# Kernel tuning notes

Measured on AMD Instinct MI355X. Metric: run time of the kernel, lower is better.

The kernel has to match this reference:

```python
import jax, jax.numpy as jnp
import numpy as np

B, T, TR, DIM, H = 1, 4096, 1024, 1536, 12
DH = DIM // H          # 128
EPS = 1e-6             # RMSNorm eps
REF_SCALE = 1.0


def setup_inputs() -> dict:
    key = jax.random.key(0)
    ks = jax.random.split(key, 20)
    s = 0.02
    w = lambda k: jax.random.normal(k, (DIM, DIM), jnp.float32) * s
    b = lambda k: jax.random.normal(k, (DIM,), jnp.float32) * 0.01
    theta = jax.random.uniform(ks[2], (T, DH // 2), jnp.float32) * (2.0 * np.pi)
    return {
        "hidden_states": jax.random.normal(ks[0], (B, T, DIM), jnp.float32),
        "ref_hidden_states": jax.random.normal(ks[1], (B, TR, DIM), jnp.float32),
        "rot_cos": jnp.cos(theta),
        "rot_sin": jnp.sin(theta),
        "Wq": w(ks[3]), "bq": b(ks[4]),
        "Wk": w(ks[5]), "bk": b(ks[6]),
        "Wv": w(ks[7]), "bv": b(ks[8]),
        "Wkr": w(ks[9]), "bkr": b(ks[10]),
        "Wvr": w(ks[11]), "bvr": b(ks[12]),
        "Wo": w(ks[13]), "bo": b(ks[14]),
        "gq": jnp.ones((DIM,), jnp.float32),
        "gk": jnp.ones((DIM,), jnp.float32),
    }


def _rmsnorm(x, g):
    return x * jax.lax.rsqrt(jnp.mean(x * x, axis=-1, keepdims=True) + EPS) * g


def _heads(x):  # [B, T, DIM] -> [B, H, T, DH]
    return x.reshape(B, -1, H, DH).transpose(0, 2, 1, 3)


def _merge(x):  # [B, H, T, DH] -> [B, T, DIM]
    return x.transpose(0, 2, 1, 3).reshape(B, -1, DIM)


def _rope(x, c, s):
    # consecutive pairs along DH form complex numbers (view_as_complex semantics)
    xe, xo = x[..., 0::2], x[..., 1::2]
    c = c[None, None]  # [1,1,T,DH/2]
    s = s[None, None]
    re = xe * c - xo * s
    im = xe * s + xo * c
    return jnp.stack([re, im], axis=-1).reshape(x.shape)


def _attn(q, k, v):
    scale = 1.0 / jnp.sqrt(jnp.asarray(DH, q.dtype))
    p = jax.nn.softmax(jnp.einsum("bhqd,bhkd->bhqk", q, k) * scale, axis=-1)
    return jnp.einsum("bhqk,bhkd->bhqd", p, v)


def reference(hidden_states, ref_hidden_states, rot_cos, rot_sin,
              Wq, bq, Wk, bk, Wv, bv, Wkr, bkr, Wvr, bvr, Wo, bo, gq, gk):
    # QKV projections (self-attention: encoder_hidden_states = hidden_states)
    q_lin = hidden_states @ Wq + bq
    k_lin = hidden_states @ Wk + bk
    v_lin = hidden_states @ Wv + bv

    # ---- reference-attention branch (uses pre-RoPE query) ----
    ref_q = _heads(_rmsnorm(q_lin, gq))
    ref_k = _heads(_rmsnorm(ref_hidden_states @ Wkr + bkr, gk))
    ref_v = _heads(ref_hidden_states @ Wvr + bvr)
    ref_out = _merge(_attn(ref_q, ref_k, ref_v))  # [B, T, DIM]

    # ---- main attention with QK-norm + RoPE ----
    q = _rope(_heads(_rmsnorm(q_lin, gq)), rot_cos, rot_sin)
    k = _rope(_heads(_rmsnorm(k_lin, gk)), rot_cos, rot_sin)
    v = _heads(v_lin)
    main_out = _merge(_attn(q, k, v))  # [B, T, DIM]

    # scaled residual combine + output projection (dropout = identity)
    out = main_out + REF_SCALE * ref_out
    return out @ Wo + bo
```

## Files before the change

kernel.cpp:

```cpp
#include <hip/hip_runtime.h>

typedef unsigned short u16;
typedef unsigned int u32;
typedef __attribute__((ext_vector_type(8))) short short8;
typedef __attribute__((ext_vector_type(4))) float f32x4;

__device__ inline u16 f2b(float f) {
  u32 u = __builtin_bit_cast(u32, f);
  u += 0x7fff + ((u >> 16) & 1);
  return (u16)(u >> 16);
}
__device__ inline float b2f(u16 u) {
  return __builtin_bit_cast(float, (u32)u << 16);
}
__device__ inline u32 pack_bf16_rn(float a, float b) {
  const u32 ua = __builtin_bit_cast(u32, a) + 0x8000u;
  const u32 ub = __builtin_bit_cast(u32, b) + 0x8000u;
  return (ua >> 16) | (ub & 0xffff0000u);
}
__device__ inline void c_store(float* p, float v) { *p = v; }
__device__ inline void c_store(u16* p, float v) { *p = f2b(v); }

__device__ inline float fexp2(float x) {
#if __has_builtin(__builtin_amdgcn_exp2f)
  return __builtin_amdgcn_exp2f(x);
#else
  return exp2f(x);
#endif
}

typedef const __attribute__((address_space(1))) u32 gu32;
typedef __attribute__((address_space(3))) u32 lu32;
__device__ inline void async16(const u16* g, u16* l) {
  __builtin_amdgcn_global_load_lds((gu32*)g, (lu32*)l, 16, 0, 0);
}

#define QS (0.08838834764831843f * 1.4426950408889634f)

template <int MI, typename TC>
__global__ __launch_bounds__(256) void gemm128_kernel(
    const u16* __restrict__ A, long lda,
    const u16* __restrict__ Bt, long ldb,
    TC* __restrict__ C0, TC* __restrict__ C1, TC* __restrict__ C2, long ldc,
    const float* b0, const float* b1, const float* b2,
    int K) {
  __shared__ u16 As[32 * MI * 32];
  __shared__ u16 Bs[128 * 32];

  const int tid = threadIdx.x;
  const int lane = tid & 63;
  const int w = tid >> 6;
  const int r = lane & 15;
  const int quad = lane >> 4;
  const int m0 = blockIdx.y * (32 * MI);
  const int nb = blockIdx.x * 128;
  const int seg = nb / 1536;
  const int nc = nb - seg * 1536;
  TC* C = seg == 0 ? C0 : (seg == 1 ? C1 : C2);
  const float* bias = seg == 0 ? b0 : (seg == 1 ? b1 : b2);

  const int srow = lane >> 2;
  const int sx = ((lane & 3) ^ (srow & 3)) * 8;
  const u16* Ag = A + (size_t)(m0 + w * 8 * MI + srow) * lda + sx;
  const u16* Bg = Bt + (size_t)(nb + w * 32 + srow) * ldb + sx;
  u16* Al[MI / 2];
#pragma unroll
  for (int j = 0; j < MI / 2; ++j) Al[j] = &As[(w * 8 * MI + 16 * j) * 32];
  u16* const Bl0 = &Bs[(w * 32) * 32];
  u16* const Bl1 = &Bs[(w * 32 + 16) * 32];

  const int wm = (w >> 1) * (16 * MI);
  const int wn = (w & 1) * 64;

  f32x4 acc[MI][4];
#pragma unroll
  for (int i = 0; i < MI; ++i)
#pragma unroll
    for (int j = 0; j < 4; ++j) acc[i][j] = (f32x4){0.f, 0.f, 0.f, 0.f};

  const int fco = (quad ^ (r & 3)) * 8;

  for (int kk = 0; kk < K; kk += 32) {
    __syncthreads();
#pragma unroll
    for (int j = 0; j < MI / 2; ++j) async16(Ag + kk + (size_t)(16 * j) * lda, Al[j]);
    async16(Bg + kk, Bl0);
    async16(Bg + kk + 16 * ldb, Bl1);
    __syncthreads();

    short8 af[MI], bf[4];
#pragma unroll
    for (int mi = 0; mi < MI; ++mi)
      af[mi] = *reinterpret_cast<const short8*>(&As[(wm + 16 * mi + r) * 32 + fco]);
#pragma unroll
    for (int ni = 0; ni < 4; ++ni)
      bf[ni] = *reinterpret_cast<const short8*>(&Bs[(wn + 16 * ni + r) * 32 + fco]);
#pragma unroll
    for (int mi = 0; mi < MI; ++mi)
#pragma unroll
      for (int ni = 0; ni < 4; ++ni)
        acc[mi][ni] = __builtin_amdgcn_mfma_f32_16x16x32_bf16(af[mi], bf[ni], acc[mi][ni], 0, 0, 0);
  }

#pragma unroll
  for (int mi = 0; mi < MI; ++mi)
#pragma unroll
    for (int ni = 0; ni < 4; ++ni)
#pragma unroll
      for (int rr = 0; rr < 4; ++rr) {
        const int row = m0 + wm + 16 * mi + 4 * quad + rr;
        const int col = nc + wn + 16 * ni + r;
        c_store(&C[(size_t)row * ldc + col], acc[mi][ni][rr] + bias[col]);
      }
}

__global__ __launch_bounds__(256) void conv2_kernel(
    const float* __restrict__ xa, u16* __restrict__ ya, int n8a,
    const float* __restrict__ xb, u16* __restrict__ yb, int n8b) {
  int i = blockIdx.x * 256 + threadIdx.x;
  const float* x;
  u16* y;
  if (i < n8a) {
    x = xa; y = ya;
  } else {
    i -= n8a;
    if (i >= n8b) return;
    x = xb; y = yb;
  }
  const float4 v0 = reinterpret_cast<const float4*>(x)[2 * i];
  const float4 v1 = reinterpret_cast<const float4*>(x)[2 * i + 1];
  uint4 rv;
  rv.x = (u32)f2b(v0.x) | ((u32)f2b(v0.y) << 16);
  rv.y = (u32)f2b(v0.z) | ((u32)f2b(v0.w) << 16);
  rv.z = (u32)f2b(v1.x) | ((u32)f2b(v1.y) << 16);
  rv.w = (u32)f2b(v1.z) | ((u32)f2b(v1.w) << 16);
  reinterpret_cast<uint4*>(y)[i] = rv;
}

__device__ inline void transconv_body(const float* __restrict__ W, u16* __restrict__ Wt) {
  __shared__ u16 Ls[64 * 72];
  const int tid = threadIdx.x;
  const int k0 = blockIdx.y * 64;
  const int n0 = blockIdx.x * 64;
#pragma unroll
  for (int i = 0; i < 4; ++i) {
    const int c = tid + 256 * i;
    const int row = c >> 4;
    const int c4 = (c & 15) * 4;
    const float4 v = *reinterpret_cast<const float4*>(&W[(size_t)(k0 + row) * 1536 + n0 + c4]);
    Ls[(c4 + 0) * 72 + row] = f2b(v.x);
    Ls[(c4 + 1) * 72 + row] = f2b(v.y);
    Ls[(c4 + 2) * 72 + row] = f2b(v.z);
    Ls[(c4 + 3) * 72 + row] = f2b(v.w);
  }
  __syncthreads();
#pragma unroll
  for (int i = 0; i < 2; ++i) {
    const int c = tid + 256 * i;
    const int n = c >> 3;
    const int kc = (c & 7) * 8;
    u16 tmp[8];
#pragma unroll
    for (int j = 0; j < 8; ++j) tmp[j] = Ls[n * 72 + kc + j];
    *reinterpret_cast<uint4*>(&Wt[(size_t)(n0 + n) * 1536 + k0 + kc]) =
        *reinterpret_cast<const uint4*>(tmp);
  }
}

__global__ __launch_bounds__(256) void transconv6_kernel(
    const float* W0, const float* W1, const float* W2,
    const float* W3, const float* W4, const float* W5,
    u16* T0, u16* T1, u16* T2, u16* T3, u16* T4, u16* T5) {
  const int z = blockIdx.z;
  const float* W = z == 0 ? W0 : z == 1 ? W1 : z == 2 ? W2 : z == 3 ? W3 : z == 4 ? W4 : W5;
  u16* Wt = z == 0 ? T0 : z == 1 ? T1 : z == 2 ? T2 : z == 3 ? T3 : z == 4 ? T4 : T5;
  transconv_body(W, Wt);
}

__global__ __launch_bounds__(256) void rmsnorm3_kernel(
    const u16* xq, const u16* xk, const u16* xkr,
    const float* gq, const float* gk,
    const float* rc, const float* rs,
    u16* oq_plain, u16* oq_rope, u16* ok_rope, u16* okr_plain) {
  __shared__ float red[4];
  const int z = blockIdx.y;
  const int row = blockIdx.x;
  if (z == 2 && row >= 1024) return;
  const u16* x; const float* g; u16* po; u16* pr; float sc;
  if (z == 0)      { x = xq;  g = gq; po = oq_plain; pr = oq_rope; sc = QS;  }
  else if (z == 1) { x = xk;  g = gk; po = nullptr;  pr = ok_rope; sc = 1.f; }
  else             { x = xkr; g = gk; po = okr_plain; pr = nullptr; sc = 1.f; }

  const int tid = threadIdx.x;
  const u32* xr = reinterpret_cast<const u32*>(x + (size_t)row * 1536);
  float xe[3], xo[3];
  float ss = 0.f;
#pragma unroll
  for (int j = 0; j < 3; ++j) {
    const u32 u = xr[tid + 256 * j];
    const float e = b2f((u16)(u & 0xffff));
    const float o = b2f((u16)(u >> 16));
    xe[j] = e; xo[j] = o;
    ss += e * e + o * o;
  }
#pragma unroll
  for (int off = 32; off; off >>= 1) ss += __shfl_xor(ss, off, 64);
  if ((tid & 63) == 0) red[tid >> 6] = ss;
  __syncthreads();
  const float total = red[0] + red[1] + red[2] + red[3];
  const float rinv = rsqrtf(total * (1.0f / 1536.0f) + 1e-6f) * sc;
  u32* po32 = po ? reinterpret_cast<u32*>(po + (size_t)row * 1536) : nullptr;
  u32* pr32 = pr ? reinterpret_cast<u32*>(pr + (size_t)row * 1536) : nullptr;
#pragma unroll
  for (int j = 0; j < 3; ++j) {
    const int p = tid + 256 * j;
    const float2 gg = reinterpret_cast<const float2*>(g)[p];
    const float e = xe[j] * rinv * gg.x;
    const float o = xo[j] * rinv * gg.y;
    if (po32) po32[p] = (u32)f2b(e) | ((u32)f2b(o) << 16);
    if (pr32) {
      const int i = p & 63;
      const float c = rc[row * 64 + i];
      const float s = rs[row * 64 + i];
      const float re = e * c - o * s;
      const float im = e * s + o * c;
      pr32[p] = (u32)f2b(re) | ((u32)f2b(im) << 16);
    }
  }
}

__global__ __launch_bounds__(256) void vtrans2_kernel(
    const u16* __restrict__ V0, u16* __restrict__ Vt0,
    const u16* __restrict__ V1, u16* __restrict__ Vt1) {
  __shared__ u16 Ls[64 * 136];
  const int z = blockIdx.z;
  const int kvLen = z == 0 ? 4096 : 1024;
  const int kv0 = blockIdx.x * 64;
  if (kv0 >= kvLen) return;
  const u16* V = z == 0 ? V0 : V1;
  u16* Vt = z == 0 ? Vt0 : Vt1;
  const int tid = threadIdx.x;
  const int h = blockIdx.y;
#pragma unroll
  for (int i = 0; i < 4; ++i) {
    const int c = tid + 256 * i;
    const int row = c >> 4, c8 = c & 15;
    *reinterpret_cast<uint4*>(&Ls[row * 136 + 8 * c8]) =
        *reinterpret_cast<const uint4*>(V + (size_t)(kv0 + row) * 1536 + h * 128 + 8 * c8);
  }
  __syncthreads();
#pragma unroll
  for (int i = 0; i < 4; ++i) {
    const int c = tid + 256 * i;
    const int d = c >> 3, kc = c & 7;
    u16 tmp[8];
#pragma unroll
    for (int j = 0; j < 8; ++j) tmp[j] = Ls[(8 * kc + j) * 136 + d];
    *reinterpret_cast<uint4*>(Vt + ((size_t)h * 128 + d) * kvLen + kv0 + 8 * kc) =
        *reinterpret_cast<const uint4*>(tmp);
  }
}

__global__ __launch_bounds__(256, 4) void flash_kernel(
    const u16* __restrict__ Qc, const u16* __restrict__ Kc,
    const u16* __restrict__ Vc, int kvLenC,
    const u16* __restrict__ Qm, const u16* __restrict__ Km,
    const u16* __restrict__ Vm, int kvLenM,
    u16* __restrict__ Ob) {
  __shared__ u16 Ks[2][32 * 128];
  __shared__ u16 Vs[2][128 * 32];
  __shared__ u16 Pb[4][16 * 40];
  __shared__ float ab[4][16];

  const int tid = threadIdx.x;
  const int lane = tid & 63;
  const int w = tid >> 6;
  const int r = lane & 15;
  const int quad = lane >> 4;
  const int h = blockIdx.y;
  const int q0 = blockIdx.x * 64;
  const int qrow = q0 + 16 * w + r;
  const int fv = (r >> 1) & 3;

  auto run_pass = [&](const u16* __restrict__ Q, const u16* __restrict__ K,
                      const u16* __restrict__ Vt, int kvLen, f32x4* Oc) {
    short8 qf[4];
    {
      const u16* qbase = Q + (size_t)qrow * 1536 + h * 128 + 8 * quad;
#pragma unroll
      for (int ks = 0; ks < 4; ++ks)
        qf[ks] = *reinterpret_cast<const short8*>(qbase + 32 * ks);
    }

    const u16* Kb = K + h * 128;
    const u16* Vb = Vt + (size_t)h * 128 * kvLen;
    u32 koff[2], voff[2];
    int klo[2], vlo[2];
    {
      const int p16 = lane & 15, rin = lane >> 4;
      const int p4 = lane & 3, din = lane >> 2;
#pragma unroll
      for (int j = 0; j < 2; ++j) {
        const int row = 8 * w + 4 * j + rin;
        koff[j] = (u32)row * 1536u + 8u * (u32)(p16 ^ (row & 15));
        klo[j] = (8 * w + 4 * j) * 128;
        const int d = 32 * w + 16 * j + din;
        voff[j] = (u32)d * (u32)kvLen + 8u * (u32)(p4 ^ ((din >> 1) & 3));
        vlo[j] = (32 * w + 16 * j) * 32;
      }
    }

#pragma unroll
    for (int dt = 0; dt < 8; ++dt) Oc[dt] = (f32x4){0.f, 0.f, 0.f, 0.f};
    float m_i = -1e30f, l_i = 0.f;

    const int nt = kvLen >> 5;

#pragma unroll
    for (int j = 0; j < 2; ++j) async16(Kb + koff[j], &Ks[0][klo[j]]);
#pragma unroll
    for (int j = 0; j < 2; ++j) async16(Vb + voff[j], &Vs[0][vlo[j]]);

    for (int t = 0; t < nt; ++t) {
      const int buf = t & 1;
      __syncthreads();
      if (t + 1 < nt) {
        const size_t ko = (size_t)(t + 1) * (32 * 1536);
        const size_t vo = (size_t)(t + 1) * 32;
#pragma unroll
        for (int j = 0; j < 2; ++j) async16(Kb + ko + koff[j], &Ks[buf ^ 1][klo[j]]);
#pragma unroll
        for (int j = 0; j < 2; ++j) async16(Vb + vo + voff[j], &Vs[buf ^ 1][vlo[j]]);
      }

      f32x4 St[2];
#pragma unroll
      for (int mt = 0; mt < 2; ++mt) St[mt] = (f32x4){0.f, 0.f, 0.f, 0.f};
      __builtin_amdgcn_s_setprio(1);
#pragma unroll
      for (int mt = 0; mt < 2; ++mt) {
        const u16* kp = &Ks[buf][(16 * mt + r) * 128];
#pragma unroll
        for (int ks = 0; ks < 4; ++ks) {
          const short8 af = *reinterpret_cast<const short8*>(kp + 8 * ((quad + 4 * ks) ^ r));
          St[mt] = __builtin_amdgcn_mfma_f32_16x16x32_bf16(af, qf[ks], St[mt], 0, 0, 0);
        }
      }
      __builtin_amdgcn_s_setprio(0);

      float mloc = -1e30f;
#pragma unroll
      for (int mt = 0; mt < 2; ++mt)
#pragma unroll
        for (int rr = 0; rr < 4; ++rr) mloc = fmaxf(mloc, St[mt][rr]);
      mloc = fmaxf(mloc, __shfl_xor(mloc, 16, 64));
      mloc = fmaxf(mloc, __shfl_xor(mloc, 32, 64));

      float alpha = 1.0f;
      if (__any(mloc > m_i + 11.5f)) {
        const float mn = fmaxf(m_i, mloc);
        alpha = fexp2(m_i - mn);
        m_i = mn;
        if (quad == 0) ab[w][r] = alpha;
        const float4 a4 = *reinterpret_cast<const float4*>(&ab[w][4 * quad]);
#pragma unroll
        for (int dt = 0; dt < 8; ++dt) {
          Oc[dt][0] *= a4.x; Oc[dt][1] *= a4.y; Oc[dt][2] *= a4.z; Oc[dt][3] *= a4.w;
        }
      }

      float psum = 0.f;
      uint2 pk[2];
#pragma unroll
      for (int mt = 0; mt < 2; ++mt) {
        const float p0 = fexp2(St[mt][0] - m_i);
        const float p1 = fexp2(St[mt][1] - m_i);
        const float p2 = fexp2(St[mt][2] - m_i);
        const float p3 = fexp2(St[mt][3] - m_i);
        psum += (p0 + p1) + (p2 + p3);
        pk[mt].x = pack_bf16_rn(p0, p1);
        pk[mt].y = pack_bf16_rn(p2, p3);
      }
      psum += __shfl_xor(psum, 16, 64);
      psum += __shfl_xor(psum, 32, 64);
      l_i = l_i * alpha + psum;

#pragma unroll
      for (int mt = 0; mt < 2; ++mt)
        *reinterpret_cast<uint2*>(&Pb[w][r * 40 + 16 * mt + 4 * quad]) = pk[mt];
      {
        const short8 pa = *reinterpret_cast<const short8*>(&Pb[w][r * 40 + 8 * quad]);
        __builtin_amdgcn_s_setprio(1);
#pragma unroll
        for (int dt = 0; dt < 8; ++dt) {
          const int d = 16 * dt + r;
          const short8 b0 = *reinterpret_cast<const short8*>(&Vs[buf][d * 32 + 8 * (quad ^ fv)]);
          Oc[dt] = __builtin_amdgcn_mfma_f32_16x16x32_bf16(pa, b0, Oc[dt], 0, 0, 0);
        }
        __builtin_amdgcn_s_setprio(0);
      }
    }

    if (quad == 0) ab[w][r] = 1.0f / l_i;
    const float4 li4 = *reinterpret_cast<const float4*>(&ab[w][4 * quad]);
#pragma unroll
    for (int dt = 0; dt < 8; ++dt) {
      Oc[dt][0] *= li4.x; Oc[dt][1] *= li4.y; Oc[dt][2] *= li4.z; Oc[dt][3] *= li4.w;
    }
  };

  f32x4 Ocr[8];
  run_pass(Qc, Kc, Vc, kvLenC, Ocr);
  __syncthreads();
  f32x4 Oc[8];
  run_pass(Qm, Km, Vm, kvLenM, Oc);

  u16* obb = Ob + (size_t)(q0 + 16 * w) * 1536 + h * 128;
#pragma unroll
  for (int rr = 0; rr < 4; ++rr) {
    u16* brow = obb + (size_t)(4 * quad + rr) * 1536 + r;
#pragma unroll
    for (int dt = 0; dt < 8; ++dt)
      brow[16 * dt] = f2b(Oc[dt][rr] + Ocr[dt][rr]);
  }
}

extern "C" void kernel_launch(void* const* d_in, const int* in_sizes, int n_in,
                              void* d_out, int out_size, void* d_ws, size_t ws_size,
                              hipStream_t stream) {
  (void)in_sizes; (void)n_in; (void)out_size; (void)ws_size;
  constexpr int T = 4096, TR = 1024, DIM = 1536, NH = 12;

  const float* hs  = (const float*)d_in[0];
  const float* rhs = (const float*)d_in[1];
  const float* rc  = (const float*)d_in[2];
  const float* rs  = (const float*)d_in[3];
  const float* Wq  = (const float*)d_in[4];
  const float* bq  = (const float*)d_in[5];
  const float* Wk  = (const float*)d_in[6];
  const float* bk  = (const float*)d_in[7];
  const float* Wv  = (const float*)d_in[8];
  const float* bv  = (const float*)d_in[9];
  const float* Wkr = (const float*)d_in[10];
  const float* bkr = (const float*)d_in[11];
  const float* Wvr = (const float*)d_in[12];
  const float* bvr = (const float*)d_in[13];
  const float* Wo  = (const float*)d_in[14];
  const float* bo  = (const float*)d_in[15];
  const float* gq  = (const float*)d_in[16];
  const float* gk  = (const float*)d_in[17];
  float* out = (float*)d_out;

  char* ws = (char*)d_ws;
  size_t off = 0;
  auto alloc = [&](size_t bytes) -> void* {
    void* p = ws + off;
    off += (bytes + 255) & ~(size_t)255;
    return p;
  };
  u16* bQ    = (u16*)alloc((size_t)T * DIM * 2);
  u16* bQr   = (u16*)alloc((size_t)T * DIM * 2);
  u16* bK    = (u16*)alloc((size_t)T * DIM * 2);
  u16* bV    = (u16*)alloc((size_t)T * DIM * 2);
  u16* bKr   = (u16*)alloc((size_t)TR * DIM * 2);
  u16* bVr   = (u16*)alloc((size_t)TR * DIM * 2);
  u16* bHs   = (u16*)alloc((size_t)T * DIM * 2);
  u16* bRhs  = (u16*)alloc((size_t)TR * DIM * 2);
  u16* bWqkv = (u16*)alloc((size_t)3 * DIM * DIM * 2);
  u16* bWr   = (u16*)alloc((size_t)2 * DIM * DIM * 2);
  u16* bWoT  = (u16*)alloc((size_t)DIM * DIM * 2);
  u16* VtG = bHs;
  u16* VtR = bRhs;
  u16* bOb = bWqkv;

  const dim3 blk(256);

  conv2_kernel<<<dim3((T * DIM / 8 + TR * DIM / 8 + 255) / 256), blk, 0, stream>>>(
      hs, bHs, T * DIM / 8, rhs, bRhs, TR * DIM / 8);

  transconv6_kernel<<<dim3(24, 24, 6), blk, 0, stream>>>(
      Wq, Wk, Wv, Wkr, Wvr, Wo,
      bWqkv + 0 * (size_t)DIM * DIM, bWqkv + 1 * (size_t)DIM * DIM,
      bWqkv + 2 * (size_t)DIM * DIM, bWr + 0 * (size_t)DIM * DIM,
      bWr + 1 * (size_t)DIM * DIM, bWoT);

  gemm128_kernel<4, u16><<<dim3(36, 32), blk, 0, stream>>>(
      bHs, DIM, bWqkv, DIM, bQ, bK, bV, DIM, bq, bk, bv, DIM);
  gemm128_kernel<2, u16><<<dim3(24, 16), blk, 0, stream>>>(
      bRhs, DIM, bWr, DIM, bKr, bVr, (u16*)nullptr, DIM, bkr, bvr, nullptr, DIM);

  rmsnorm3_kernel<<<dim3(T, 3), blk, 0, stream>>>(
      bQ, bK, bKr, gq, gk, rc, rs, bQ, bQr, bK, bKr);

  vtrans2_kernel<<<dim3(T / 64, NH, 2), blk, 0, stream>>>(bV, VtG, bVr, VtR);

  flash_kernel<<<dim3(T / 64, NH), blk, 0, stream>>>(
      bQ, bKr, VtR, TR, bQr, bK, VtG, T, bOb);

  gemm128_kernel<2, float><<<dim3(12, 64), blk, 0, stream>>>(
      bOb, DIM, bWoT, DIM, out, (float*)nullptr, (float*)nullptr, DIM, bo, nullptr, nullptr, DIM);
}
```

Baseline: 542.6 us.

## Process two query tiles per wave in flash kernel with 128-thread blocks

The flash attention block shrinks from four waves to two, and each wave now handles 32 query rows (two 16-row tiles). Each K/V fragment read from shared memory then feeds two MFMAs, which halves LDS traffic per unit of compute. The first pass writes its fp32 output to a new global scratch buffer, and the second pass reads it back to combine. This replaces holding two register accumulator sets and frees registers for the doubled tile. The cost is fewer waves per block, more global memory traffic for the fp32 intermediate, and more per-thread async loads.

```diff
diff --git a/kernel.cpp b/kernel.cpp
--- a/kernel.cpp
+++ b/kernel.cpp
@@ -261,15 +261,15 @@
   }
 }
 
-__global__ __launch_bounds__(256, 4) void flash_kernel(
+__global__ __launch_bounds__(128, 2) void flash_kernel(
     const u16* __restrict__ Qc, const u16* __restrict__ Kc,
     const u16* __restrict__ Vc, int kvLenC,
     const u16* __restrict__ Qm, const u16* __restrict__ Km,
     const u16* __restrict__ Vm, int kvLenM,
-    u16* __restrict__ Ob) {
+    float* __restrict__ O, u16* __restrict__ Ob) {
   __shared__ u16 Ks[2][32 * 128];
   __shared__ u16 Vs[2][128 * 32];
-  __shared__ u16 Pb[4][16 * 40];
+  __shared__ u16 Pb[2][32 * 40];
   __shared__ float ab[4][16];
 
   const int tid = threadIdx.x;
@@ -279,47 +279,50 @@
   const int quad = lane >> 4;
   const int h = blockIdx.y;
   const int q0 = blockIdx.x * 64;
-  const int qrow = q0 + 16 * w + r;
   const int fv = (r >> 1) & 3;
 
   auto run_pass = [&](const u16* __restrict__ Q, const u16* __restrict__ K,
-                      const u16* __restrict__ Vt, int kvLen, f32x4* Oc) {
-    short8 qf[4];
-    {
-      const u16* qbase = Q + (size_t)qrow * 1536 + h * 128 + 8 * quad;
+                      const u16* __restrict__ Vt, int kvLen, bool addO) {
+    short8 qf[2][4];
+#pragma unroll
+    for (int qt = 0; qt < 2; ++qt) {
+      const u16* qbase = Q + (size_t)(q0 + 32 * w + 16 * qt + r) * 1536 + h * 128 + 8 * quad;
 #pragma unroll
       for (int ks = 0; ks < 4; ++ks)
-        qf[ks] = *reinterpret_cast<const short8*>(qbase + 32 * ks);
+        qf[qt][ks] = *reinterpret_cast<const short8*>(qbase + 32 * ks);
     }
 
     const u16* Kb = K + h * 128;
     const u16* Vb = Vt + (size_t)h * 128 * kvLen;
-    u32 koff[2], voff[2];
-    int klo[2], vlo[2];
+    u32 koff[4], voff[4];
+    int klo[4], vlo[4];
     {
       const int p16 = lane & 15, rin = lane >> 4;
       const int p4 = lane & 3, din = lane >> 2;
 #pragma unroll
-      for (int j = 0; j < 2; ++j) {
-        const int row = 8 * w + 4 * j + rin;
+      for (int j = 0; j < 4; ++j) {
+        const int row = 16 * w + 4 * j + rin;
         koff[j] = (u32)row * 1536u + 8u * (u32)(p16 ^ (row & 15));
-        klo[j] = (8 * w + 4 * j) * 128;
-        const int d = 32 * w + 16 * j + din;
-        voff[j] = (u32)d * (u32)kvLen + 8u * (u32)(p4 ^ ((din >> 1) & 3));
-        vlo[j] = (32 * w + 16 * j) * 32;
+        klo[j] = (16 * w + 4 * j) * 128;
+        const int d = 64 * w + 16 * j + din;
+        voff[j] = (u32)d * (u32)kvLen + 8u * (u32)(p4 ^ ((d >> 1) & 3));
+        vlo[j] = (64 * w + 16 * j) * 32;
       }
     }
 
-#pragma unroll
-    for (int dt = 0; dt < 8; ++dt) Oc[dt] = (f32x4){0.f, 0.f, 0.f, 0.f};
-    float m_i = -1e30f, l_i = 0.f;
+    f32x4 Oc[2][8];
+#pragma unroll
+    for (int qt = 0; qt < 2; ++qt)
+#pragma unroll
+      for (int dt = 0; dt < 8; ++dt) Oc[qt][dt] = (f32x4){0.f, 0.f, 0.f, 0.f};
+    float m_i[2] = {-1e30f, -1e30f}, l_i[2] = {0.f, 0.f};
 
     const int nt = kvLen >> 5;
 
 #pragma unroll
-    for (int j = 0; j < 2; ++j) async16(Kb + koff[j], &Ks[0][klo[j]]);
-#pragma unroll
-    for (int j = 0; j < 2; ++j) async16(Vb + voff[j], &Vs[0][vlo[j]]);
+    for (int j = 0; j < 4; ++j) async16(Kb + koff[j], &Ks[0][klo[j]]);
+#pragma unroll
+    for (int j = 0; j < 4; ++j) async16(Vb + voff[j], &Vs[0][vlo[j]]);
 
     for (int t = 0; t < nt; ++t) {
       const int buf = t & 1;
@@ -328,14 +331,16 @@
         const size_t ko = (size_t)(t + 1) * (32 * 1536);
         const size_t vo = (size_t)(t + 1) * 32;
 #pragma unroll
-        for (int j = 0; j < 2; ++j) async16(Kb + ko + koff[j], &Ks[buf ^ 1][klo[j]]);
-#pragma unroll
-        for (int j = 0; j < 2; ++j) async16(Vb + vo + voff[j], &Vs[buf ^ 1][vlo[j]]);
-      }
-
-      f32x4 St[2];
-#pragma unroll
-      for (int mt = 0; mt < 2; ++mt) St[mt] = (f32x4){0.f, 0.f, 0.f, 0.f};
+        for (int j = 0; j < 4; ++j) async16(Kb + ko + koff[j], &Ks[buf ^ 1][klo[j]]);
+#pragma unroll
+        for (int j = 0; j < 4; ++j) async16(Vb + vo + voff[j], &Vs[buf ^ 1][vlo[j]]);
+      }
+
+      f32x4 St[2][2];
+#pragma unroll
+      for (int qt = 0; qt < 2; ++qt)
+#pragma unroll
+        for (int mt = 0; mt < 2; ++mt) St[qt][mt] = (f32x4){0.f, 0.f, 0.f, 0.f};
       __builtin_amdgcn_s_setprio(1);
 #pragma unroll
       for (int mt = 0; mt < 2; ++mt) {
@@ -343,86 +348,106 @@
 #pragma unroll
         for (int ks = 0; ks < 4; ++ks) {
           const short8 af = *reinterpret_cast<const short8*>(kp + 8 * ((quad + 4 * ks) ^ r));
-          St[mt] = __builtin_amdgcn_mfma_f32_16x16x32_bf16(af, qf[ks], St[mt], 0, 0, 0);
+#pragma unroll
+          for (int qt = 0; qt < 2; ++qt)
+            St[qt][mt] = __builtin_amdgcn_mfma_f32_16x16x32_bf16(af, qf[qt][ks], St[qt][mt], 0, 0, 0);
         }
       }
       __builtin_amdgcn_s_setprio(0);
 
-      float mloc = -1e30f;
-#pragma unroll
-      for (int mt = 0; mt < 2; ++mt)
-#pragma unroll
-        for (int rr = 0; rr < 4; ++rr) mloc = fmaxf(mloc, St[mt][rr]);
-      mloc = fmaxf(mloc, __shfl_xor(mloc, 16, 64));
-      mloc = fmaxf(mloc, __shfl_xor(mloc, 32, 64));
-
-      float alpha = 1.0f;
-      if (__any(mloc > m_i + 11.5f)) {
-        const float mn = fmaxf(m_i, mloc);
-        alpha = fexp2(m_i - mn);
-        m_i = mn;
-        if (quad == 0) ab[w][r] = alpha;
-        const float4 a4 = *reinterpret_cast<const float4*>(&ab[w][4 * quad]);
-#pragma unroll
-        for (int dt = 0; dt < 8; ++dt) {
-          Oc[dt][0] *= a4.x; Oc[dt][1] *= a4.y; Oc[dt][2] *= a4.z; Oc[dt][3] *= a4.w;
+      uint2 pk[2][2];
+#pragma unroll
+      for (int qt = 0; qt < 2; ++qt) {
+        float mloc = -1e30f;
+#pragma unroll
+        for (int mt = 0; mt < 2; ++mt)
+#pragma unroll
+          for (int rr = 0; rr < 4; ++rr) mloc = fmaxf(mloc, St[qt][mt][rr]);
+        mloc = fmaxf(mloc, __shfl_xor(mloc, 16, 64));
+        mloc = fmaxf(mloc, __shfl_xor(mloc, 32, 64));
+
+        float alpha = 1.0f;
+        if (__any(mloc > m_i[qt] + 11.5f)) {
+          const float mn = fmaxf(m_i[qt], mloc);
+          alpha = fexp2(m_i[qt] - mn);
+          m_i[qt] = mn;
+          if (quad == 0) ab[2 * w + qt][r] = alpha;
+          const float4 a4 = *reinterpret_cast<const float4*>(&ab[2 * w + qt][4 * quad]);
+#pragma unroll
+          for (int dt = 0; dt < 8; ++dt) {
+            Oc[qt][dt][0] *= a4.x; Oc[qt][dt][1] *= a4.y;
+            Oc[qt][dt][2] *= a4.z; Oc[qt][dt][3] *= a4.w;
+          }
         }
-      }
-
-      float psum = 0.f;
-      uint2 pk[2];
-#pragma unroll
-      for (int mt = 0; mt < 2; ++mt) {
-        const float p0 = fexp2(St[mt][0] - m_i);
-        const float p1 = fexp2(St[mt][1] - m_i);
-        const float p2 = fexp2(St[mt][2] - m_i);
-        const float p3 = fexp2(St[mt][3] - m_i);
-        psum += (p0 + p1) + (p2 + p3);
-        pk[mt].x = pack_bf16_rn(p0, p1);
-        pk[mt].y = pack_bf16_rn(p2, p3);
-      }
-      psum += __shfl_xor(psum, 16, 64);
-      psum += __shfl_xor(psum, 32, 64);
-      l_i = l_i * alpha + psum;
-
-#pragma unroll
-      for (int mt = 0; mt < 2; ++mt)
-        *reinterpret_cast<uint2*>(&Pb[w][r * 40 + 16 * mt + 4 * quad]) = pk[mt];
+
+        float psum = 0.f;
+#pragma unroll
+        for (int mt = 0; mt < 2; ++mt) {
+          const float p0 = fexp2(St[qt][mt][0] - m_i[qt]);
+          const float p1 = fexp2(St[qt][mt][1] - m_i[qt]);
+          const float p2 = fexp2(St[qt][mt][2] - m_i[qt]);
+          const float p3 = fexp2(St[qt][mt][3] - m_i[qt]);
+          psum += (p0 + p1) + (p2 + p3);
+          pk[qt][mt].x = pack_bf16_rn(p0, p1);
+          pk[qt][mt].y = pack_bf16_rn(p2, p3);
+        }
+        psum += __shfl_xor(psum, 16, 64);
+        psum += __shfl_xor(psum, 32, 64);
+        l_i[qt] = l_i[qt] * alpha + psum;
+      }
+
+#pragma unroll
+      for (int qt = 0; qt < 2; ++qt)
+#pragma unroll
+        for (int mt = 0; mt < 2; ++mt)
+          *reinterpret_cast<uint2*>(&Pb[w][(16 * qt + r) * 40 + 16 * mt + 4 * quad]) = pk[qt][mt];
       {
-        const short8 pa = *reinterpret_cast<const short8*>(&Pb[w][r * 40 + 8 * quad]);
+        short8 pa[2];
+#pragma unroll
+        for (int qt = 0; qt < 2; ++qt)
+          pa[qt] = *reinterpret_cast<const short8*>(&Pb[w][(16 * qt + r) * 40 + 8 * quad]);
         __builtin_amdgcn_s_setprio(1);
 #pragma unroll
         for (int dt = 0; dt < 8; ++dt) {
           const int d = 16 * dt + r;
           const short8 b0 = *reinterpret_cast<const short8*>(&Vs[buf][d * 32 + 8 * (quad ^ fv)]);
-          Oc[dt] = __builtin_amdgcn_mfma_f32_16x16x32_bf16(pa, b0, Oc[dt], 0, 0, 0);
+#pragma unroll
+          for (int qt = 0; qt < 2; ++qt)
+            Oc[qt][dt] = __builtin_amdgcn_mfma_f32_16x16x32_bf16(pa[qt], b0, Oc[qt][dt], 0, 0, 0);
         }
         __builtin_amdgcn_s_setprio(0);
       }
     }
 
-    if (quad == 0) ab[w][r] = 1.0f / l_i;
-    const float4 li4 = *reinterpret_cast<const float4*>(&ab[w][4 * quad]);
-#pragma unroll
-    for (int dt = 0; dt < 8; ++dt) {
-      Oc[dt][0] *= li4.x; Oc[dt][1] *= li4.y; Oc[dt][2] *= li4.z; Oc[dt][3] *= li4.w;
+#pragma unroll
+    for (int qt = 0; qt < 2; ++qt) {
+      if (quad == 0) ab[2 * w + qt][r] = 1.0f / l_i[qt];
+      const float4 li4 = *reinterpret_cast<const float4*>(&ab[2 * w + qt][4 * quad]);
+      const float lv[4] = {li4.x, li4.y, li4.z, li4.w};
+      const int rowb = q0 + 32 * w + 16 * qt;
+      float* obf = O + (size_t)rowb * 1536 + h * 128;
+      u16* obb = Ob + (size_t)rowb * 1536 + h * 128;
+#pragma unroll
+      for (int rr = 0; rr < 4; ++rr) {
+        float* orow = obf + (size_t)(4 * quad + rr) * 1536 + r;
+        u16* brow = obb + (size_t)(4 * quad + rr) * 1536 + r;
+#pragma unroll
+        for (int dt = 0; dt < 8; ++dt) {
+          float v = Oc[qt][dt][rr] * lv[rr];
+          if (addO) {
+            v += orow[16 * dt];
+            brow[16 * dt] = f2b(v);
+          } else {
+            orow[16 * dt] = v;
+          }
+        }
+      }
     }
   };
 
-  f32x4 Ocr[8];
-  run_pass(Qc, Kc, Vc, kvLenC, Ocr);
+  run_pass(Qc, Kc, Vc, kvLenC, false);
   __syncthreads();
-  f32x4 Oc[8];
-  run_pass(Qm, Km, Vm, kvLenM, Oc);
-
-  u16* obb = Ob + (size_t)(q0 + 16 * w) * 1536 + h * 128;
-#pragma unroll
-  for (int rr = 0; rr < 4; ++rr) {
-    u16* brow = obb + (size_t)(4 * quad + rr) * 1536 + r;
-#pragma unroll
-    for (int dt = 0; dt < 8; ++dt)
-      brow[16 * dt] = f2b(Oc[dt][rr] + Ocr[dt][rr]);
-  }
+  run_pass(Qm, Km, Vm, kvLenM, true);
 }
 
 extern "C" void kernel_launch(void* const* d_in, const int* in_sizes, int n_in,
@@ -464,6 +489,7 @@
   u16* bV    = (u16*)alloc((size_t)T * DIM * 2);
   u16* bKr   = (u16*)alloc((size_t)TR * DIM * 2);
   u16* bVr   = (u16*)alloc((size_t)TR * DIM * 2);
+  float* bO  = (float*)alloc((size_t)T * DIM * 4);
   u16* bHs   = (u16*)alloc((size_t)T * DIM * 2);
   u16* bRhs  = (u16*)alloc((size_t)TR * DIM * 2);
   u16* bWqkv = (u16*)alloc((size_t)3 * DIM * DIM * 2);
@@ -494,8 +520,8 @@
 
   vtrans2_kernel<<<dim3(T / 64, NH, 2), blk, 0, stream>>>(bV, VtG, bVr, VtR);
 
-  flash_kernel<<<dim3(T / 64, NH), blk, 0, stream>>>(
-      bQ, bKr, VtR, TR, bQr, bK, VtG, T, bOb);
+  flash_kernel<<<dim3(T / 64, NH), dim3(128), 0, stream>>>(
+      bQ, bKr, VtR, TR, bQr, bK, VtG, T, bO, bOb);
 
   gemm128_kernel<2, float><<<dim3(12, 64), blk, 0, stream>>>(
       bOb, DIM, bWoT, DIM, out, (float*)nullptr, (float*)nullptr, DIM, bo, nullptr, nullptr, DIM);
```

Result: slower. 581.7 us (+7.2%).
